# Performance work log

Measured on AMD Instinct MI355X. Metric: run time of the kernel, lower is better.

The kernel has to match this reference:

```python
import jax, jax.numpy as jnp
import numpy as np

D_MODEL = 1024
N_HEADS = 16
HEAD_DIM = D_MODEL // N_HEADS
ROPE_DIM = HEAD_DIM  # rope_fraction=1.0
BASE = 10000.0


def _rope_cos_sin(T, dtype):
    theta = 1.0 / (BASE ** (jnp.arange(0, ROPE_DIM, 2, dtype=jnp.float32) / ROPE_DIM))
    t = jnp.arange(T, dtype=jnp.float32)
    freqs = jnp.outer(t, theta)                     # [T, ROPE_DIM/2]
    emb = jnp.concatenate([freqs, freqs], axis=-1)  # [T, ROPE_DIM]
    return jnp.cos(emb).astype(dtype), jnp.sin(emb).astype(dtype)


def _rotate(x, cos, sin):
    # x: [B, H, T, D]; apply rotary to first ROPE_DIM dims (here full D)
    x_rope, x_pass = x[..., :ROPE_DIM], x[..., ROPE_DIM:]
    x1, x2 = x_rope[..., :ROPE_DIM // 2], x_rope[..., ROPE_DIM // 2:]
    rotated = jnp.concatenate([-x2, x1], axis=-1)
    x_rope = x_rope * cos + rotated * sin
    return jnp.concatenate([x_rope, x_pass], axis=-1)


def setup_inputs() -> dict:
    key = jax.random.key(0)
    k1, k2, k3 = jax.random.split(key, 3)
    x = jax.random.normal(k1, (4, 2048, D_MODEL), dtype=jnp.float32)
    w_qkv = jax.random.normal(k2, (3 * D_MODEL, D_MODEL), dtype=jnp.float32) * (1.0 / np.sqrt(D_MODEL))
    w_out = jax.random.normal(k3, (D_MODEL, D_MODEL), dtype=jnp.float32) * (1.0 / np.sqrt(D_MODEL))
    return {"x": x, "w_qkv": w_qkv, "w_out": w_out}


def reference(x, w_qkv, w_out):
    B, T, C = x.shape
    qkv = jnp.einsum('btc,oc->bto', x, w_qkv)  # Linear: x @ W.T
    q, k, v = jnp.split(qkv, 3, axis=-1)

    def reshape(t):
        return t.reshape(B, T, N_HEADS, HEAD_DIM).transpose(0, 2, 1, 3)  # [B,H,T,D]

    q, k, v = reshape(q), reshape(k), reshape(v)

    cos, sin = _rope_cos_sin(T, x.dtype)  # [T, ROPE_DIM]
    cos = cos[None, None, :, :]
    sin = sin[None, None, :, :]
    q = _rotate(q, cos, sin)
    k = _rotate(k, cos, sin)

    scale = 1.0 / np.sqrt(HEAD_DIM).astype(np.float32)
    attn = jnp.einsum('bhqd,bhkd->bhqk', q, k) * scale
    causal = jnp.tril(jnp.ones((T, T), dtype=bool))
    attn = jnp.where(causal[None, None], attn, jnp.finfo(attn.dtype).min)
    attn = jax.nn.softmax(attn, axis=-1)
    out = jnp.einsum('bhqk,bhkd->bhqd', attn, v)
    out = out.transpose(0, 2, 1, 3).reshape(B, T, C)
    return jnp.einsum('btc,oc->bto', out, w_out)
```

## Files before the change

### kernel.cpp

```cpp
#include <hip/hip_runtime.h>

typedef unsigned short u16;
typedef __attribute__((ext_vector_type(8))) short v8s;
typedef __attribute__((ext_vector_type(4))) float v4f;

__device__ __forceinline__ u16 f2bf(float f) {
  unsigned u = __float_as_uint(f);
  u += 0x7FFF + ((u >> 16) & 1);
  return (u16)(u >> 16);
}

__device__ __forceinline__ unsigned pk2bf(float lo, float hi) {
  unsigned a = __float_as_uint(lo) + 0x8000u;
  unsigned b = __float_as_uint(hi) + 0x8000u;
  return __builtin_amdgcn_perm(b, a, 0x07060302);
}

__device__ __forceinline__ v4f zero4() {
  v4f z; z[0] = 0.f; z[1] = 0.f; z[2] = 0.f; z[3] = 0.f; return z;
}

__device__ __forceinline__ void async16(const u16* g, u16* l) {
  __builtin_amdgcn_global_load_lds(
      (const __attribute__((address_space(1))) unsigned int*)g,
      (__attribute__((address_space(3))) unsigned int*)l, 16, 0, 0);
}

__device__ __forceinline__ void fast_sincos(float x, float* s, float* c) {
  float k = rintf(x * 0.15915494309189535f);
  float r = __builtin_fmaf(k, -6.28125f, x);
  r = __builtin_fmaf(k, -0.0019353071795864769f, r);
  *s = __sinf(r);
  *c = __cosf(r);
}

#define ATTN_SCL (0.125f * 1.4426950408889634f)

__global__ __launch_bounds__(256) void cast_bf16_k(const float* __restrict__ s,
                                                   u16* __restrict__ d, int n4) {
  int i = blockIdx.x * 256 + threadIdx.x;
  if (i >= n4) return;
  float4 v = ((const float4*)s)[i];
  ((ushort4*)d)[i] = make_ushort4(f2bf(v.x), f2bf(v.y), f2bf(v.z), f2bf(v.w));
}


__device__ __forceinline__ void gemm_core(const u16* __restrict__ A,
                                          const u16* __restrict__ B, int K,
                                          int row0, int col0, u16* As, u16* Bs,
                                          v4f acc[4][4]) {
  const int tid = threadIdx.x;
  const int lane = tid & 63;
  const int wm = (tid >> 7) & 1;
  const int wn = (tid >> 6) & 1;
  const int ln = lane & 15, quad = lane >> 4;
#pragma unroll
  for (int i = 0; i < 4; ++i)
#pragma unroll
    for (int j = 0; j < 4; ++j) acc[i][j] = zero4();
  const int rA = tid >> 3;
  const int cA = (((tid & 7) ^ (rA & 7)) << 3);
  for (int kt = 0; kt < K; kt += 64) {
#pragma unroll
    for (int i = 0; i < 4; ++i) {
      async16(A + (size_t)(row0 + i * 32 + rA) * K + kt + cA, As + i * 2048 + tid * 8);
      async16(B + (size_t)(col0 + i * 32 + rA) * K + kt + cA, Bs + i * 2048 + tid * 8);
    }
    __syncthreads();
#pragma unroll
    for (int kk = 0; kk < 2; ++kk) {
      const int go = (((kk * 4 + quad) ^ (ln & 7)) << 3);
      v8s af[4], bfr[4];
#pragma unroll
      for (int i = 0; i < 4; ++i) {
        af[i]  = *(const v8s*)(As + (wm * 64 + i * 16 + ln) * 64 + go);
        bfr[i] = *(const v8s*)(Bs + (wn * 64 + i * 16 + ln) * 64 + go);
      }
      __builtin_amdgcn_s_setprio(1);
#pragma unroll
      for (int i = 0; i < 4; ++i)
#pragma unroll
        for (int j = 0; j < 4; ++j)
          acc[i][j] = __builtin_amdgcn_mfma_f32_16x16x32_bf16(af[i], bfr[j], acc[i][j], 0, 0, 0);
      __builtin_amdgcn_s_setprio(0);
    }
    __syncthreads();
  }
}

__global__ __launch_bounds__(256) void gemm_qkv_rope(const u16* __restrict__ A,
                                                     const u16* __restrict__ B,
                                                     u16* __restrict__ Qh,
                                                     u16* __restrict__ Kh,
                                                     u16* __restrict__ Vt) {
  __shared__ __align__(16) u16 As[8192];
  __shared__ __align__(16) u16 Bs[8192];
  v4f acc[4][4];
  const int row0 = blockIdx.x * 128, col0 = blockIdx.y * 128;
  gemm_core(A, B, 1024, row0, col0, As, Bs, acc);
  const int tid = threadIdx.x, lane = tid & 63;
  const int wm = (tid >> 7) & 1, wn = (tid >> 6) & 1;
  const int ln = lane & 15, quad = lane >> 4;
  const int colbase = col0 + wn * 64;
  const int seg = colbase >> 10;
  const int h = (colbase & 1023) >> 6;
  if (seg < 2) {
    u16* dst = (seg == 0) ? Qh : Kh;
    const float oscl = (seg == 0) ? ATTN_SCL : 1.0f;
#pragma unroll
    for (int i = 0; i < 4; ++i) {
#pragma unroll
      for (int r = 0; r < 4; ++r) {
        int row = row0 + wm * 64 + i * 16 + quad * 4 + r;
        int b = row >> 11, t = row & 2047;
        size_t base = ((size_t)(b * 16 + h) * 2048 + t) * 64;
#pragma unroll
        for (int j = 0; j < 2; ++j) {
          int d1 = j * 16 + ln;
          float theta = exp2f((float)d1 * -0.4152410118609203f);
          float sn, cs;
          fast_sincos((float)t * theta, &sn, &cs);
          float v1 = acc[i][j][r], v2 = acc[i][j + 2][r];
          dst[base + d1]      = f2bf((v1 * cs - v2 * sn) * oscl);
          dst[base + d1 + 32] = f2bf((v2 * cs + v1 * sn) * oscl);
        }
      }
    }
  } else {
#pragma unroll
    for (int i = 0; i < 4; ++i)
#pragma unroll
      for (int j = 0; j < 4; ++j) {
        int d = j * 16 + ln;
#pragma unroll
        for (int r = 0; r < 4; ++r) {
          int row = row0 + wm * 64 + i * 16 + quad * 4 + r;
          int b = row >> 11, t = row & 2047;
          Vt[((size_t)(b * 16 + h) * 64 + d) * 2048 + t] = f2bf(acc[i][j][r]);
        }
      }
  }
}

__global__ __launch_bounds__(256, 4) void gemm_out_k(const u16* __restrict__ A,
                                                     const u16* __restrict__ B,
                                                     float* __restrict__ C) {
  __shared__ __align__(16) u16 As[128 * 64];
  __shared__ __align__(16) u16 Bs[64 * 64];
  const int tid = threadIdx.x;
  const int lane = tid & 63;
  const int wm = (tid >> 7) & 1;
  const int wn = (tid >> 6) & 1;
  const int ln = lane & 15, quad = lane >> 4;
  const int row0 = blockIdx.x * 128, col0 = blockIdx.y * 64;
  const int K = 1024;
  v4f acc[4][2];
#pragma unroll
  for (int i = 0; i < 4; ++i)
#pragma unroll
    for (int j = 0; j < 2; ++j) acc[i][j] = zero4();
  const int rA = tid >> 3;
  const int cA = (((tid & 7) ^ (rA & 7)) << 3);
  for (int kt = 0; kt < K; kt += 64) {
#pragma unroll
    for (int i = 0; i < 4; ++i)
      async16(A + (size_t)(row0 + i * 32 + rA) * K + kt + cA, As + i * 2048 + tid * 8);
#pragma unroll
    for (int i = 0; i < 2; ++i)
      async16(B + (size_t)(col0 + i * 32 + rA) * K + kt + cA, Bs + i * 2048 + tid * 8);
    __syncthreads();
#pragma unroll
    for (int kk = 0; kk < 2; ++kk) {
      const int go = (((kk * 4 + quad) ^ (ln & 7)) << 3);
      v8s af[4], bfr[2];
#pragma unroll
      for (int i = 0; i < 4; ++i)
        af[i] = *(const v8s*)(As + (wm * 64 + i * 16 + ln) * 64 + go);
#pragma unroll
      for (int j = 0; j < 2; ++j)
        bfr[j] = *(const v8s*)(Bs + (wn * 32 + j * 16 + ln) * 64 + go);
      __builtin_amdgcn_s_setprio(1);
#pragma unroll
      for (int i = 0; i < 4; ++i)
#pragma unroll
        for (int j = 0; j < 2; ++j)
          acc[i][j] = __builtin_amdgcn_mfma_f32_16x16x32_bf16(af[i], bfr[j], acc[i][j], 0, 0, 0);
      __builtin_amdgcn_s_setprio(0);
    }
    __syncthreads();
  }
#pragma unroll
  for (int i = 0; i < 4; ++i)
#pragma unroll
    for (int r = 0; r < 4; ++r) {
      int row = row0 + wm * 64 + i * 16 + quad * 4 + r;
#pragma unroll
      for (int j = 0; j < 2; ++j) {
        int col = col0 + wn * 32 + j * 16 + ln;
        C[(size_t)row * 1024 + col] = acc[i][j][r];
      }
    }
}


template <bool MASKED>
__device__ __forceinline__ void flash_tile64(const u16* Ks, const u16* Vs, u16* Pw,
                                             const v8s aq[2], v4f od[4], float& l,
                                             int s0, int qrow, int ln, int quad,
                                             int swz) {
  v4f sc[4];
#pragma unroll
  for (int kf = 0; kf < 4; ++kf) sc[kf] = zero4();
#pragma unroll
  for (int kk = 0; kk < 2; ++kk) {
    const int go = (((kk * 4 + quad) ^ (ln & 7)) << 3);
    __builtin_amdgcn_s_setprio(1);
#pragma unroll
    for (int kf = 0; kf < 4; ++kf) {
      v8s ak = *(const v8s*)(Ks + (kf * 16 + ln) * 64 + go);
      sc[kf] = __builtin_amdgcn_mfma_f32_16x16x32_bf16(ak, aq[kk], sc[kf], 0, 0, 0);
    }
    __builtin_amdgcn_s_setprio(0);
  }
  float ls = 0.f;
#pragma unroll
  for (int kf = 0; kf < 4; ++kf) {
    float p[4];
#pragma unroll
    for (int r = 0; r < 4; ++r) {
      float v = sc[kf][r];
      if (MASKED) {
        int key = s0 + kf * 16 + quad * 4 + r;
        v = (key <= qrow) ? v : -3.0e38f;
      }
      p[r] = exp2f(v);
    }
    ls += (p[0] + p[1]) + (p[2] + p[3]);
    uint2 pk;
    pk.x = pk2bf(p[0], p[1]);
    pk.y = pk2bf(p[2], p[3]);
    *(uint2*)(Pw + ln * 64 + (((kf * 4 + quad) ^ swz) << 2)) = pk;
  }
  l += ls;
#pragma unroll
  for (int kk = 0; kk < 2; ++kk) {
    v8s bp = *(const v8s*)(Pw + ln * 64 + (((kk * 8 + quad * 2) ^ swz) << 2));
    const int go = (((kk * 4 + quad) ^ (ln & 7)) << 3);
    __builtin_amdgcn_s_setprio(1);
#pragma unroll
    for (int df = 0; df < 4; ++df) {
      v8s av = *(const v8s*)(Vs + (df * 16 + ln) * 64 + go);
      od[df] = __builtin_amdgcn_mfma_f32_16x16x32_bf16(av, bp, od[df], 0, 0, 0);
    }
    __builtin_amdgcn_s_setprio(0);
  }
}

__global__ __launch_bounds__(256, 4) void flash_k(const u16* __restrict__ Q,
                                                  const u16* __restrict__ Kh,
                                                  const u16* __restrict__ V,
                                                  u16* __restrict__ O) {
  __shared__ __align__(16) u16 Ks[2][4096];
  __shared__ __align__(16) u16 Vs[2][4096];
  __shared__ __align__(16) u16 Ps[4096];
  const int tid = threadIdx.x;
  const int lane = tid & 63, w = tid >> 6;
  const int ln = lane & 15, quad = lane >> 4;
  const int swz = (lane & 7) << 1;
  const int bx = blockIdx.y;
  const int bh = blockIdx.x;
  const int b = bh >> 4, h = bh & 15;
  const size_t qoff = (size_t)bh * 2048 * 64;
  u16* Pw = Ps + w * 1024;

  const int rS = tid >> 3;
  const int cS = (((tid & 7) ^ (rS & 7)) << 3);
  const u16* Kbase = Kh + qoff;
  const u16* Vbase = V + (size_t)bh * 131072;

#pragma unroll
  for (int ph = 0; ph < 2; ++ph) {
    const int qt_idx = ph ? bx : 31 - bx;
    const int q0 = qt_idx * 64 + w * 16;
    const int qrow = q0 + ln;
    v8s aq[2];
#pragma unroll
    for (int kk = 0; kk < 2; ++kk)
      aq[kk] = *(const v8s*)(Q + qoff + (size_t)(q0 + ln) * 64 + kk * 32 + quad * 8);
    float l = 0.f;
    v4f od[4];
#pragma unroll
    for (int df = 0; df < 4; ++df) od[df] = zero4();

    const int nt = qt_idx + 1;
    {
      async16(Kbase + (size_t)rS * 64 + cS, Ks[0] + tid * 8);
      async16(Kbase + (size_t)(32 + rS) * 64 + cS, Ks[0] + 2048 + tid * 8);
      async16(Vbase + (size_t)rS * 2048 + cS, Vs[0] + tid * 8);
      async16(Vbase + (size_t)(rS + 32) * 2048 + cS, Vs[0] + 2048 + tid * 8);
    }
    for (int it = 0; it < nt; ++it) {
      __syncthreads();
      if (it + 1 < nt) {
        const int s1 = (it + 1) * 64;
        u16* kd = Ks[(it + 1) & 1];
        u16* vd = Vs[(it + 1) & 1];
        async16(Kbase + (size_t)(s1 + rS) * 64 + cS, kd + tid * 8);
        async16(Kbase + (size_t)(s1 + 32 + rS) * 64 + cS, kd + 2048 + tid * 8);
        async16(Vbase + (size_t)rS * 2048 + s1 + cS, vd + tid * 8);
        async16(Vbase + (size_t)(rS + 32) * 2048 + s1 + cS, vd + 2048 + tid * 8);
      }
      const int s0 = it * 64;
      if (it == nt - 1)
        flash_tile64<true>(Ks[it & 1], Vs[it & 1], Pw, aq, od, l, s0, qrow, ln, quad, swz);
      else
        flash_tile64<false>(Ks[it & 1], Vs[it & 1], Pw, aq, od, l, s0, qrow, ln, quad, swz);
    }
    __syncthreads();

    float lt = l;
    lt += __shfl_xor(lt, 16);
    lt += __shfl_xor(lt, 32);
    float inv = 1.0f / lt;
    int t = q0 + ln;
    size_t obase = ((size_t)b * 2048 + t) * 1024 + h * 64;
#pragma unroll
    for (int df = 0; df < 4; ++df) {
      ushort4 o;
      o.x = f2bf(od[df][0] * inv);
      o.y = f2bf(od[df][1] * inv);
      o.z = f2bf(od[df][2] * inv);
      o.w = f2bf(od[df][3] * inv);
      *(ushort4*)(O + obase + df * 16 + quad * 4) = o;
    }
  }
}

extern "C" void kernel_launch(void* const* d_in, const int* in_sizes, int n_in,
                              void* d_out, int out_size, void* d_ws, size_t ws_size,
                              hipStream_t stream) {
  const float* x     = (const float*)d_in[0];
  const float* w_qkv = (const float*)d_in[1];
  const float* w_out = (const float*)d_in[2];
  float* out = (float*)d_out;
  char* ws = (char*)d_ws;
  u16* xb    = (u16*)(ws);
  u16* wqkvb = (u16*)(ws + 16777216);
  u16* woutb = (u16*)(ws + 23068672);
  u16* qh    = (u16*)(ws + 25165824);
  u16* kh    = (u16*)(ws + 41943040);
  u16* vt    = (u16*)(ws + 58720256);
  u16* oa    = (u16*)(ws + 75497472);

  cast_bf16_k<<<8192, 256, 0, stream>>>(x, xb, 2097152);
  cast_bf16_k<<<3072, 256, 0, stream>>>(w_qkv, wqkvb, 786432);
  cast_bf16_k<<<1024, 256, 0, stream>>>(w_out, woutb, 262144);
  gemm_qkv_rope<<<dim3(64, 24), 256, 0, stream>>>(xb, wqkvb, qh, kh, vt);
  flash_k<<<dim3(64, 16), 256, 0, stream>>>(qh, kh, vt, oa);
  gemm_out_k<<<dim3(64, 16), 256, 0, stream>>>(oa, woutb, out);
}
```

Baseline: 250.1 us.

## Share K/V tiles across paired query tiles in flash kernel; fuse cast launches

The flash kernel used to process its two query tiles (31-bx and bx) one after the other, loading K/V twice. It now streams K/V once for the longer tile and applies each loaded tile to both query tiles while the shorter one is still active, roughly halving K/V global traffic for the second tile. The three fp32-to-bf16 cast launches are merged into one kernel that picks its source by index, since the workspace offsets are contiguous. Holding two sets of accumulators and Q fragments raises register pressure under launch_bounds(256,4) and may cause spills. The imbalance in work per iteration also changes between iterations.

```diff
diff --git a/kernel.cpp b/kernel.cpp
--- a/kernel.cpp
+++ b/kernel.cpp
@@ -36,12 +36,18 @@
 
 #define ATTN_SCL (0.125f * 1.4426950408889634f)
 
-__global__ __launch_bounds__(256) void cast_bf16_k(const float* __restrict__ s,
-                                                   u16* __restrict__ d, int n4) {
+__global__ __launch_bounds__(256) void cast_all_k(const float* __restrict__ x,
+                                                  const float* __restrict__ wq,
+                                                  const float* __restrict__ wo,
+                                                  u16* __restrict__ dst) {
   int i = blockIdx.x * 256 + threadIdx.x;
-  if (i >= n4) return;
-  float4 v = ((const float4*)s)[i];
-  ((ushort4*)d)[i] = make_ushort4(f2bf(v.x), f2bf(v.y), f2bf(v.z), f2bf(v.w));
+  const float4* s;
+  int si;
+  if (i < 2097152) { s = (const float4*)x;  si = i; }
+  else if (i < 2883584) { s = (const float4*)wq; si = i - 2097152; }
+  else { s = (const float4*)wo; si = i - 2883584; }
+  float4 v = s[si];
+  ((ushort4*)dst)[i] = make_ushort4(f2bf(v.x), f2bf(v.y), f2bf(v.z), f2bf(v.w));
 }
 
 
@@ -256,6 +262,26 @@
   }
 }
 
+__device__ __forceinline__ void flash_epilogue(float l, const v4f od[4], int q0,
+                                               int b, int h, int ln, int quad,
+                                               u16* __restrict__ O) {
+  float lt = l;
+  lt += __shfl_xor(lt, 16);
+  lt += __shfl_xor(lt, 32);
+  float inv = 1.0f / lt;
+  int t = q0 + ln;
+  size_t obase = ((size_t)b * 2048 + t) * 1024 + h * 64;
+#pragma unroll
+  for (int df = 0; df < 4; ++df) {
+    ushort4 o;
+    o.x = f2bf(od[df][0] * inv);
+    o.y = f2bf(od[df][1] * inv);
+    o.z = f2bf(od[df][2] * inv);
+    o.w = f2bf(od[df][3] * inv);
+    *(ushort4*)(O + obase + df * 16 + quad * 4) = o;
+  }
+}
+
 __global__ __launch_bounds__(256, 4) void flash_k(const u16* __restrict__ Q,
                                                   const u16* __restrict__ Kh,
                                                   const u16* __restrict__ V,
@@ -278,62 +304,55 @@
   const u16* Kbase = Kh + qoff;
   const u16* Vbase = V + (size_t)bh * 131072;
 
-#pragma unroll
-  for (int ph = 0; ph < 2; ++ph) {
-    const int qt_idx = ph ? bx : 31 - bx;
-    const int q0 = qt_idx * 64 + w * 16;
-    const int qrow = q0 + ln;
-    v8s aq[2];
-#pragma unroll
-    for (int kk = 0; kk < 2; ++kk)
-      aq[kk] = *(const v8s*)(Q + qoff + (size_t)(q0 + ln) * 64 + kk * 32 + quad * 8);
-    float l = 0.f;
-    v4f od[4];
-#pragma unroll
-    for (int df = 0; df < 4; ++df) od[df] = zero4();
-
-    const int nt = qt_idx + 1;
-    {
-      async16(Kbase + (size_t)rS * 64 + cS, Ks[0] + tid * 8);
-      async16(Kbase + (size_t)(32 + rS) * 64 + cS, Ks[0] + 2048 + tid * 8);
-      async16(Vbase + (size_t)rS * 2048 + cS, Vs[0] + tid * 8);
-      async16(Vbase + (size_t)(rS + 32) * 2048 + cS, Vs[0] + 2048 + tid * 8);
-    }
-    for (int it = 0; it < nt; ++it) {
-      __syncthreads();
-      if (it + 1 < nt) {
-        const int s1 = (it + 1) * 64;
-        u16* kd = Ks[(it + 1) & 1];
-        u16* vd = Vs[(it + 1) & 1];
-        async16(Kbase + (size_t)(s1 + rS) * 64 + cS, kd + tid * 8);
-        async16(Kbase + (size_t)(s1 + 32 + rS) * 64 + cS, kd + 2048 + tid * 8);
-        async16(Vbase + (size_t)rS * 2048 + s1 + cS, vd + tid * 8);
-        async16(Vbase + (size_t)(rS + 32) * 2048 + s1 + cS, vd + 2048 + tid * 8);
-      }
-      const int s0 = it * 64;
-      if (it == nt - 1)
-        flash_tile64<true>(Ks[it & 1], Vs[it & 1], Pw, aq, od, l, s0, qrow, ln, quad, swz);
+  const int qtA = 31 - bx, qtB = bx;
+  const int ntA = qtA + 1, ntB = qtB + 1;
+  const int q0A = qtA * 64 + w * 16, q0B = qtB * 64 + w * 16;
+  const int qrowA = q0A + ln, qrowB = q0B + ln;
+  v8s aqA[2], aqB[2];
+#pragma unroll
+  for (int kk = 0; kk < 2; ++kk) {
+    aqA[kk] = *(const v8s*)(Q + qoff + (size_t)(q0A + ln) * 64 + kk * 32 + quad * 8);
+    aqB[kk] = *(const v8s*)(Q + qoff + (size_t)(q0B + ln) * 64 + kk * 32 + quad * 8);
+  }
+  float lA = 0.f, lB = 0.f;
+  v4f odA[4], odB[4];
+#pragma unroll
+  for (int df = 0; df < 4; ++df) { odA[df] = zero4(); odB[df] = zero4(); }
+
+  {
+    async16(Kbase + (size_t)rS * 64 + cS, Ks[0] + tid * 8);
+    async16(Kbase + (size_t)(32 + rS) * 64 + cS, Ks[0] + 2048 + tid * 8);
+    async16(Vbase + (size_t)rS * 2048 + cS, Vs[0] + tid * 8);
+    async16(Vbase + (size_t)(rS + 32) * 2048 + cS, Vs[0] + 2048 + tid * 8);
+  }
+  for (int it = 0; it < ntA; ++it) {
+    __syncthreads();
+    if (it + 1 < ntA) {
+      const int s1 = (it + 1) * 64;
+      u16* kd = Ks[(it + 1) & 1];
+      u16* vd = Vs[(it + 1) & 1];
+      async16(Kbase + (size_t)(s1 + rS) * 64 + cS, kd + tid * 8);
+      async16(Kbase + (size_t)(s1 + 32 + rS) * 64 + cS, kd + 2048 + tid * 8);
+      async16(Vbase + (size_t)rS * 2048 + s1 + cS, vd + tid * 8);
+      async16(Vbase + (size_t)(rS + 32) * 2048 + s1 + cS, vd + 2048 + tid * 8);
+    }
+    const int s0 = it * 64;
+    const u16* Kc = Ks[it & 1];
+    const u16* Vc = Vs[it & 1];
+    if (it == ntA - 1)
+      flash_tile64<true>(Kc, Vc, Pw, aqA, odA, lA, s0, qrowA, ln, quad, swz);
+    else
+      flash_tile64<false>(Kc, Vc, Pw, aqA, odA, lA, s0, qrowA, ln, quad, swz);
+    if (it < ntB) {
+      if (it == ntB - 1)
+        flash_tile64<true>(Kc, Vc, Pw, aqB, odB, lB, s0, qrowB, ln, quad, swz);
       else
-        flash_tile64<false>(Ks[it & 1], Vs[it & 1], Pw, aq, od, l, s0, qrow, ln, quad, swz);
-    }
-    __syncthreads();
-
-    float lt = l;
-    lt += __shfl_xor(lt, 16);
-    lt += __shfl_xor(lt, 32);
-    float inv = 1.0f / lt;
-    int t = q0 + ln;
-    size_t obase = ((size_t)b * 2048 + t) * 1024 + h * 64;
-#pragma unroll
-    for (int df = 0; df < 4; ++df) {
-      ushort4 o;
-      o.x = f2bf(od[df][0] * inv);
-      o.y = f2bf(od[df][1] * inv);
-      o.z = f2bf(od[df][2] * inv);
-      o.w = f2bf(od[df][3] * inv);
-      *(ushort4*)(O + obase + df * 16 + quad * 4) = o;
-    }
-  }
+        flash_tile64<false>(Kc, Vc, Pw, aqB, odB, lB, s0, qrowB, ln, quad, swz);
+    }
+  }
+
+  flash_epilogue(lA, odA, q0A, b, h, ln, quad, O);
+  flash_epilogue(lB, odB, q0B, b, h, ln, quad, O);
 }
 
 extern "C" void kernel_launch(void* const* d_in, const int* in_sizes, int n_in,
@@ -352,9 +371,7 @@
   u16* vt    = (u16*)(ws + 58720256);
   u16* oa    = (u16*)(ws + 75497472);
 
-  cast_bf16_k<<<8192, 256, 0, stream>>>(x, xb, 2097152);
-  cast_bf16_k<<<3072, 256, 0, stream>>>(w_qkv, wqkvb, 786432);
-  cast_bf16_k<<<1024, 256, 0, stream>>>(w_out, woutb, 262144);
+  cast_all_k<<<12288, 256, 0, stream>>>(x, w_qkv, w_out, (u16*)ws);
   gemm_qkv_rope<<<dim3(64, 24), 256, 0, stream>>>(xb, wqkvb, qh, kh, vt);
   flash_k<<<dim3(64, 16), 256, 0, stream>>>(qh, kh, vt, oa);
   gemm_out_k<<<dim3(64, 16), 256, 0, stream>>>(oa, woutb, out);
```

Result: slower. 302.9 us (+21.1%).

## Merge cast kernels and run both flash query tiles concurrently in 512-thread blocks

Applied to the files above, without the earlier changes.

The three fp32-to-bf16 cast launches become one kernel that indexes into x, w_qkv and w_out by range and writes into the contiguous workspace. The flash kernel no longer processes its two paired query tiles (long and short) one after the other with 256 threads. It now uses 512 threads, with one 4-wave group per tile, and the groups share a single K/V tile stream that runs over the longer tile's range. Each thread loads half as much K/V per step, the Ps buffer doubles, and the second pass over the short tile's K/V range goes away. The cost is that the short-tile group sits idle while the long tile finishes, and the bigger block may change occupancy.

```diff
diff --git a/kernel.cpp b/kernel.cpp
--- a/kernel.cpp
+++ b/kernel.cpp
@@ -36,12 +36,18 @@
 
 #define ATTN_SCL (0.125f * 1.4426950408889634f)
 
-__global__ __launch_bounds__(256) void cast_bf16_k(const float* __restrict__ s,
-                                                   u16* __restrict__ d, int n4) {
+__global__ __launch_bounds__(256) void cast_all_k(const float* __restrict__ x,
+                                                  const float* __restrict__ wq,
+                                                  const float* __restrict__ wo,
+                                                  u16* __restrict__ dst) {
   int i = blockIdx.x * 256 + threadIdx.x;
-  if (i >= n4) return;
-  float4 v = ((const float4*)s)[i];
-  ((ushort4*)d)[i] = make_ushort4(f2bf(v.x), f2bf(v.y), f2bf(v.z), f2bf(v.w));
+  const float4* s;
+  int si;
+  if (i < 2097152) { s = (const float4*)x;  si = i; }
+  else if (i < 2883584) { s = (const float4*)wq; si = i - 2097152; }
+  else { s = (const float4*)wo; si = i - 2883584; }
+  float4 v = s[si];
+  ((ushort4*)dst)[i] = make_ushort4(f2bf(v.x), f2bf(v.y), f2bf(v.z), f2bf(v.w));
 }
 
 
@@ -256,15 +262,16 @@
   }
 }
 
-__global__ __launch_bounds__(256, 4) void flash_k(const u16* __restrict__ Q,
+__global__ __launch_bounds__(512, 6) void flash_k(const u16* __restrict__ Q,
                                                   const u16* __restrict__ Kh,
                                                   const u16* __restrict__ V,
                                                   u16* __restrict__ O) {
   __shared__ __align__(16) u16 Ks[2][4096];
   __shared__ __align__(16) u16 Vs[2][4096];
-  __shared__ __align__(16) u16 Ps[4096];
+  __shared__ __align__(16) u16 Ps[8192];
   const int tid = threadIdx.x;
   const int lane = tid & 63, w = tid >> 6;
+  const int g = w >> 2, wl = w & 3;
   const int ln = lane & 15, quad = lane >> 4;
   const int swz = (lane & 7) << 1;
   const int bx = blockIdx.y;
@@ -278,61 +285,53 @@
   const u16* Kbase = Kh + qoff;
   const u16* Vbase = V + (size_t)bh * 131072;
 
-#pragma unroll
-  for (int ph = 0; ph < 2; ++ph) {
-    const int qt_idx = ph ? bx : 31 - bx;
-    const int q0 = qt_idx * 64 + w * 16;
-    const int qrow = q0 + ln;
-    v8s aq[2];
-#pragma unroll
-    for (int kk = 0; kk < 2; ++kk)
-      aq[kk] = *(const v8s*)(Q + qoff + (size_t)(q0 + ln) * 64 + kk * 32 + quad * 8);
-    float l = 0.f;
-    v4f od[4];
-#pragma unroll
-    for (int df = 0; df < 4; ++df) od[df] = zero4();
-
-    const int nt = qt_idx + 1;
-    {
-      async16(Kbase + (size_t)rS * 64 + cS, Ks[0] + tid * 8);
-      async16(Kbase + (size_t)(32 + rS) * 64 + cS, Ks[0] + 2048 + tid * 8);
-      async16(Vbase + (size_t)rS * 2048 + cS, Vs[0] + tid * 8);
-      async16(Vbase + (size_t)(rS + 32) * 2048 + cS, Vs[0] + 2048 + tid * 8);
-    }
-    for (int it = 0; it < nt; ++it) {
-      __syncthreads();
-      if (it + 1 < nt) {
-        const int s1 = (it + 1) * 64;
-        u16* kd = Ks[(it + 1) & 1];
-        u16* vd = Vs[(it + 1) & 1];
-        async16(Kbase + (size_t)(s1 + rS) * 64 + cS, kd + tid * 8);
-        async16(Kbase + (size_t)(s1 + 32 + rS) * 64 + cS, kd + 2048 + tid * 8);
-        async16(Vbase + (size_t)rS * 2048 + s1 + cS, vd + tid * 8);
-        async16(Vbase + (size_t)(rS + 32) * 2048 + s1 + cS, vd + 2048 + tid * 8);
-      }
+  const int qt = g ? bx : 31 - bx;
+  const int nt = qt + 1;
+  const int ntA = 32 - bx;
+  const int q0 = qt * 64 + wl * 16;
+  const int qrow = q0 + ln;
+  v8s aq[2];
+#pragma unroll
+  for (int kk = 0; kk < 2; ++kk)
+    aq[kk] = *(const v8s*)(Q + qoff + (size_t)(q0 + ln) * 64 + kk * 32 + quad * 8);
+  float l = 0.f;
+  v4f od[4];
+#pragma unroll
+  for (int df = 0; df < 4; ++df) od[df] = zero4();
+
+  async16(Kbase + (size_t)rS * 64 + cS, Ks[0] + tid * 8);
+  async16(Vbase + (size_t)rS * 2048 + cS, Vs[0] + tid * 8);
+
+  for (int it = 0; it < ntA; ++it) {
+    __syncthreads();
+    if (it + 1 < ntA) {
+      const int s1 = (it + 1) * 64;
+      async16(Kbase + (size_t)(s1 + rS) * 64 + cS, Ks[(it + 1) & 1] + tid * 8);
+      async16(Vbase + (size_t)rS * 2048 + s1 + cS, Vs[(it + 1) & 1] + tid * 8);
+    }
+    if (it < nt) {
       const int s0 = it * 64;
       if (it == nt - 1)
         flash_tile64<true>(Ks[it & 1], Vs[it & 1], Pw, aq, od, l, s0, qrow, ln, quad, swz);
       else
         flash_tile64<false>(Ks[it & 1], Vs[it & 1], Pw, aq, od, l, s0, qrow, ln, quad, swz);
     }
-    __syncthreads();
-
-    float lt = l;
-    lt += __shfl_xor(lt, 16);
-    lt += __shfl_xor(lt, 32);
-    float inv = 1.0f / lt;
-    int t = q0 + ln;
-    size_t obase = ((size_t)b * 2048 + t) * 1024 + h * 64;
-#pragma unroll
-    for (int df = 0; df < 4; ++df) {
-      ushort4 o;
-      o.x = f2bf(od[df][0] * inv);
-      o.y = f2bf(od[df][1] * inv);
-      o.z = f2bf(od[df][2] * inv);
-      o.w = f2bf(od[df][3] * inv);
-      *(ushort4*)(O + obase + df * 16 + quad * 4) = o;
-    }
+  }
+
+  float lt = l;
+  lt += __shfl_xor(lt, 16);
+  lt += __shfl_xor(lt, 32);
+  float inv = 1.0f / lt;
+  int t = q0 + ln;
+  size_t obase = ((size_t)b * 2048 + t) * 1024 + h * 64;
+#pragma unroll
+  for (int df = 0; df < 4; ++df) {
+    ushort4 o;
+    o.x = f2bf(od[df][0] * inv);
+    o.y = f2bf(od[df][1] * inv);
+    o.z = f2bf(od[df][2] * inv);
+    o.w = f2bf(od[df][3] * inv);
+    *(ushort4*)(O + obase + df * 16 + quad * 4) = o;
   }
 }
 
@@ -352,10 +351,8 @@
   u16* vt    = (u16*)(ws + 58720256);
   u16* oa    = (u16*)(ws + 75497472);
 
-  cast_bf16_k<<<8192, 256, 0, stream>>>(x, xb, 2097152);
-  cast_bf16_k<<<3072, 256, 0, stream>>>(w_qkv, wqkvb, 786432);
-  cast_bf16_k<<<1024, 256, 0, stream>>>(w_out, woutb, 262144);
+  cast_all_k<<<12288, 256, 0, stream>>>(x, w_qkv, w_out, (u16*)ws);
   gemm_qkv_rope<<<dim3(64, 24), 256, 0, stream>>>(xb, wqkvb, qh, kh, vt);
-  flash_k<<<dim3(64, 16), 256, 0, stream>>>(qh, kh, vt, oa);
+  flash_k<<<dim3(64, 16), 512, 0, stream>>>(qh, kh, vt, oa);
   gemm_out_k<<<dim3(64, 16), 256, 0, stream>>>(oa, woutb, out);
 }
```

Result: slower. 266.9 us (+6.7%).
